# Kernel tuning notes

Measured on AMD Instinct MI355X. Metric: run time of the kernel, lower is better.

The kernel has to match this reference:

```python
import jax, jax.numpy as jnp
import numpy as np

H = 8              # n_heads
N_PER_GRAPH = 64   # nodes per graph (equal-sized graphs)


def setup_inputs() -> dict:
    key = jax.random.key(0)
    ks = jax.random.split(key, 5)
    total, D = 65536, 512
    x = jax.random.normal(ks[0], (total, D), dtype=jnp.float32)
    batch = jnp.arange(total, dtype=jnp.int64) // N_PER_GRAPH  # sorted graph ids
    s = 1.0 / np.sqrt(D).astype(np.float32)
    # nn.MultiheadAttention packed in-proj (xavier-ish uniform) + zero bias
    in_proj_w = jax.random.uniform(ks[1], (3 * D, D), jnp.float32, -s, s)
    in_proj_b = jnp.zeros((3 * D,), jnp.float32)
    out_proj_w = jax.random.uniform(ks[2], (D, D), jnp.float32, -s, s)
    out_proj_b = jnp.zeros((D,), jnp.float32)
    gate_w = jax.random.uniform(ks[3], (1, D), jnp.float32, -s, s)
    gate_b = jnp.zeros((1,), jnp.float32)
    return {"x": x, "batch": batch, "in_proj_w": in_proj_w, "in_proj_b": in_proj_b,
            "out_proj_w": out_proj_w, "out_proj_b": out_proj_b,
            "gate_w": gate_w, "gate_b": gate_b}


def reference(x, batch, in_proj_w, in_proj_b, out_proj_w, out_proj_b, gate_w, gate_b):
    total, D = x.shape
    G = total // N_PER_GRAPH
    hd = D // H
    xg = x.reshape(G, N_PER_GRAPH, D)                       # [G, N, D]
    # packed qkv projection (torch: x @ in_proj_w.T + in_proj_b)
    qkv = jnp.einsum('gnd,ed->gne', xg, in_proj_w) + in_proj_b
    q, k, v = jnp.split(qkv, 3, axis=-1)
    def to_heads(t):
        return t.reshape(G, N_PER_GRAPH, H, hd).transpose(0, 2, 1, 3)  # [G, H, N, hd]
    q, k, v = to_heads(q), to_heads(k), to_heads(v)
    scores = jnp.einsum('ghnd,ghmd->ghnm', q, k) * (1.0 / np.sqrt(hd))
    attn = jax.nn.softmax(scores, axis=-1)
    ctx = jnp.einsum('ghnm,ghmd->ghnd', attn, v)
    ctx = ctx.transpose(0, 2, 1, 3).reshape(G, N_PER_GRAPH, D)
    attn_out = jnp.einsum('gnd,ed->gne', ctx, out_proj_w) + out_proj_b  # [G, N, D]
    gates = jax.nn.sigmoid(jnp.einsum('gnd,od->gno', attn_out, gate_w) + gate_b)
    return (attn_out * gates).sum(axis=1)                   # [G, D]
```

## Files before the change

### kernel.cpp

```cpp
#include <hip/hip_runtime.h>
#include <stdint.h>


typedef __attribute__((ext_vector_type(8))) short short8;
typedef __attribute__((ext_vector_type(4))) float f32x4;

#define D_ 512

#define WQKV_OFF   0u
#define WO_OFF     1572864u
#define UPART_OFF  2097152u
#define U_OFF      2129920u
#define C0_OFF     2131968u
#define SG_OFF     2132032u
#define WCTX_OFF   2136128u

__device__ __forceinline__ unsigned short f2bf(float f) {
    union { float f; unsigned int u; } t; t.f = f;
    unsigned int u = t.u;
    return (unsigned short)((u + 0x7FFFu + ((u >> 16) & 1u)) >> 16);
}
__device__ __forceinline__ unsigned pack2(float a, float b) {
    return (unsigned)f2bf(a) | ((unsigned)f2bf(b) << 16);
}

__global__ __launch_bounds__(256)
void convert_weights(const float* __restrict__ wqkv, const float* __restrict__ wo,
                     unsigned short* __restrict__ wbf) {
    const int i4 = blockIdx.x * 256 + threadIdx.x;
    float4 v;
    if (i4 < 196608) v = *(const float4*)(wqkv + (size_t)i4 * 4);
    else             v = *(const float4*)(wo   + (size_t)(i4 - 196608) * 4);
    uint2 p; p.x = pack2(v.x, v.y); p.y = pack2(v.z, v.w);
    *(uint2*)(wbf + (size_t)i4 * 4) = p;
}

__global__ __launch_bounds__(256)
void compute_u_partial(const float* __restrict__ wo, const float* __restrict__ gw,
                       float* __restrict__ upart) {
    const int b = blockIdx.x;
    const int t = threadIdx.x;
    float a0 = 0.f, a1 = 0.f;
    #pragma unroll 4
    for (int e = b * 32; e < b * 32 + 32; ++e) {
        const float ge = gw[e];
        a0 += wo[(size_t)e * 512 + t]       * ge;
        a1 += wo[(size_t)e * 512 + t + 256] * ge;
    }
    upart[b * 512 + t] = a0; upart[b * 512 + t + 256] = a1;
}

__global__ __launch_bounds__(256)
void finalize_u(const float* __restrict__ upart, const float* __restrict__ bo,
                const float* __restrict__ gw, const float* __restrict__ gb,
                float* __restrict__ u, float* __restrict__ c0) {
    const int t = threadIdx.x;
    float s0 = 0.f, s1 = 0.f;
    #pragma unroll
    for (int b = 0; b < 16; ++b) { s0 += upart[b*512 + t]; s1 += upart[b*512 + t + 256]; }
    u[t] = s0; u[t + 256] = s1;
    __shared__ float rb[256];
    rb[t] = bo[t] * gw[t] + bo[t + 256] * gw[t + 256];
    __syncthreads();
    for (int s = 128; s > 0; s >>= 1) { if (t < s) rb[t] += rb[t + s]; __syncthreads(); }
    if (t == 0) c0[0] = rb[0] + gb[0];
}

union U8 { unsigned u[4]; short8 s; };

__global__ __launch_bounds__(512, 2)
void attn_ctx_kernel(const float* __restrict__ x,
                     const unsigned short* __restrict__ wqkv,
                     const float* __restrict__ bqkv,
                     const float* __restrict__ u,
                     const float* __restrict__ c0,
                     unsigned short* __restrict__ wctx_ws,
                     float* __restrict__ sumgate)
{
    __shared__ unsigned short xs[64][520];
    __shared__ unsigned short scr[8][64][72];
    __shared__ float logitp[8][64];
    __shared__ float gatev[64];

    const int g    = blockIdx.x;
    const int tid  = threadIdx.x;
    const int w    = tid >> 6;
    const int lane = tid & 63;
    const int l15  = lane & 15;
    const int quad = lane >> 4;

    #pragma unroll
    for (int i = 0; i < 16; ++i) {
        int idx = tid + i * 512;
        int row = idx >> 7;
        int c4  = idx & 127;
        float4 v = *(const float4*)(x + ((size_t)(g*64 + row))*512 + c4*4);
        uint2 p; p.x = pack2(v.x, v.y); p.y = pack2(v.z, v.w);
        *(uint2*)(&xs[row][c4*4]) = p;
    }
    __syncthreads();

    const int h = w;
    unsigned short (*S)[72] = scr[w];

    U8 qA[4][2], kB[4][2];
    #pragma unroll
    for (int dt = 0; dt < 4; ++dt) {
        f32x4 aq[4], ak[4], av[4];
        #pragma unroll
        for (int nt = 0; nt < 4; ++nt) {
            aq[nt] = (f32x4){0.f,0.f,0.f,0.f};
            ak[nt] = (f32x4){0.f,0.f,0.f,0.f};
            av[nt] = (f32x4){0.f,0.f,0.f,0.f};
        }
        const unsigned short* wq = wqkv + (size_t)(          h*64 + dt*16 + l15) * 512;
        const unsigned short* wk = wqkv + (size_t)( 512 +    h*64 + dt*16 + l15) * 512;
        const unsigned short* wv = wqkv + (size_t)(1024 +    h*64 + dt*16 + l15) * 512;
        #pragma unroll 4
        for (int ks = 0; ks < 16; ++ks) {
            const int col = ks*32 + quad*8;
            short8 a0 = *(const short8*)(wq + col);
            short8 a1 = *(const short8*)(wk + col);
            short8 a2 = *(const short8*)(wv + col);
            #pragma unroll
            for (int nt = 0; nt < 4; ++nt) {
                short8 b = *(const short8*)(&xs[nt*16 + l15][col]);
                aq[nt] = __builtin_amdgcn_mfma_f32_16x16x32_bf16(a0, b, aq[nt], 0,0,0);
                ak[nt] = __builtin_amdgcn_mfma_f32_16x16x32_bf16(a1, b, ak[nt], 0,0,0);
                av[nt] = __builtin_amdgcn_mfma_f32_16x16x32_bf16(a2, b, av[nt], 0,0,0);
            }
        }
        float bq[4], bk2[4], bv2[4];
        #pragma unroll
        for (int r = 0; r < 4; ++r) {
            bq[r]  = bqkv[          h*64 + dt*16 + quad*4 + r];
            bk2[r] = bqkv[ 512 +    h*64 + dt*16 + quad*4 + r];
            bv2[r] = bqkv[1024 +    h*64 + dt*16 + quad*4 + r];
        }
        const bool take = ((quad >> 1) == (dt & 1));
        const int  ks2  = dt >> 1;
        #pragma unroll
        for (int nt = 0; nt < 4; ++nt) {
            unsigned q01 = pack2(aq[nt][0]+bq[0],  aq[nt][1]+bq[1]);
            unsigned q23 = pack2(aq[nt][2]+bq[2],  aq[nt][3]+bq[3]);
            unsigned k01 = pack2(ak[nt][0]+bk2[0], ak[nt][1]+bk2[1]);
            unsigned k23 = pack2(ak[nt][2]+bk2[2], ak[nt][3]+bk2[3]);
            #pragma unroll
            for (int j = 0; j < 4; ++j) {
                int srcl = ((quad & 1)*2 + (j >> 1))*16 + l15;
                unsigned tq = (unsigned)__shfl((int)((j & 1) ? q23 : q01), srcl);
                unsigned tk = (unsigned)__shfl((int)((j & 1) ? k23 : k01), srcl);
                if (take) { qA[nt][ks2].u[j] = tq; kB[nt][ks2].u[j] = tk; }
            }
            #pragma unroll
            for (int r = 0; r < 4; ++r)
                S[dt*16 + quad*4 + r][nt*16 + l15] = f2bf(av[nt][r] + bv2[r]);
        }
    }

    f32x4 sacc[4][4];
    #pragma unroll
    for (int a = 0; a < 4; ++a)
        #pragma unroll
        for (int b = 0; b < 4; ++b) sacc[a][b] = (f32x4){0.f,0.f,0.f,0.f};
    #pragma unroll
    for (int ks2 = 0; ks2 < 2; ++ks2)
        #pragma unroll
        for (int a = 0; a < 4; ++a)
            #pragma unroll
            for (int b = 0; b < 4; ++b)
                sacc[a][b] = __builtin_amdgcn_mfma_f32_16x16x32_bf16(
                                 qA[a][ks2].s, kB[b][ks2].s, sacc[a][b], 0,0,0);

    #pragma unroll
    for (int a = 0; a < 4; ++a) {
        #pragma unroll
        for (int r = 0; r < 4; ++r) {
            float m0 = -1e30f;
            #pragma unroll
            for (int b = 0; b < 4; ++b) { sacc[a][b][r] *= 0.125f; m0 = fmaxf(m0, sacc[a][b][r]); }
            m0 = fmaxf(m0, __shfl_xor(m0, 1));
            m0 = fmaxf(m0, __shfl_xor(m0, 2));
            m0 = fmaxf(m0, __shfl_xor(m0, 4));
            m0 = fmaxf(m0, __shfl_xor(m0, 8));
            float s = 0.f;
            #pragma unroll
            for (int b = 0; b < 4; ++b) { float e = __expf(sacc[a][b][r] - m0); sacc[a][b][r] = e; s += e; }
            s += __shfl_xor(s, 1); s += __shfl_xor(s, 2); s += __shfl_xor(s, 4); s += __shfl_xor(s, 8);
            float inv = 1.0f / s;
            #pragma unroll
            for (int b = 0; b < 4; ++b) sacc[a][b][r] *= inv;
        }
    }

    U8 vA[4][2];
    #pragma unroll
    for (int dtile = 0; dtile < 4; ++dtile)
        #pragma unroll
        for (int ks2 = 0; ks2 < 2; ++ks2)
            vA[dtile][ks2].s = *(const short8*)(&S[dtile*16 + l15][ks2*32 + quad*8]);

    #pragma unroll
    for (int a = 0; a < 4; ++a)
        #pragma unroll
        for (int b = 0; b < 4; ++b)
            #pragma unroll
            for (int r = 0; r < 4; ++r)
                S[a*16 + quad*4 + r][b*16 + l15] = f2bf(sacc[a][b][r]);

    U8 pB[4][2];
    #pragma unroll
    for (int a = 0; a < 4; ++a)
        #pragma unroll
        for (int ks2 = 0; ks2 < 2; ++ks2)
            pB[a][ks2].s = *(const short8*)(&S[a*16 + l15][ks2*32 + quad*8]);

    f32x4 cacc[4][4];
    #pragma unroll
    for (int dtile = 0; dtile < 4; ++dtile)
        #pragma unroll
        for (int a = 0; a < 4; ++a) cacc[dtile][a] = (f32x4){0.f,0.f,0.f,0.f};
    #pragma unroll
    for (int ks2 = 0; ks2 < 2; ++ks2)
        #pragma unroll
        for (int dtile = 0; dtile < 4; ++dtile)
            #pragma unroll
            for (int a = 0; a < 4; ++a)
                cacc[dtile][a] = __builtin_amdgcn_mfma_f32_16x16x32_bf16(
                                     vA[dtile][ks2].s, pB[a][ks2].s, cacc[dtile][a], 0,0,0);

    {
        float uv[4][4];
        #pragma unroll
        for (int dtile = 0; dtile < 4; ++dtile)
            #pragma unroll
            for (int r = 0; r < 4; ++r)
                uv[dtile][r] = u[h*64 + dtile*16 + quad*4 + r];
        #pragma unroll
        for (int a = 0; a < 4; ++a) {
            float s = 0.f;
            #pragma unroll
            for (int dtile = 0; dtile < 4; ++dtile)
                #pragma unroll
                for (int r = 0; r < 4; ++r)
                    s += cacc[dtile][a][r] * uv[dtile][r];
            s += __shfl_xor(s, 16); s += __shfl_xor(s, 32);
            if (quad == 0) logitp[w][a*16 + l15] = s;
        }
    }
    __syncthreads();

    if (tid < 64) {
        float lg = c0[0];
        #pragma unroll
        for (int ww = 0; ww < 8; ++ww) lg += logitp[ww][tid];
        float gt = 1.0f / (1.0f + __expf(-lg));
        gatev[tid] = gt;
        float s = gt;
        s += __shfl_xor(s, 1);  s += __shfl_xor(s, 2);  s += __shfl_xor(s, 4);
        s += __shfl_xor(s, 8);  s += __shfl_xor(s, 16); s += __shfl_xor(s, 32);
        if (tid == 0) sumgate[g] = s;
    }
    __syncthreads();

    {
        float gv[4];
        #pragma unroll
        for (int a = 0; a < 4; ++a) gv[a] = gatev[a*16 + l15];
        #pragma unroll
        for (int dtile = 0; dtile < 4; ++dtile) {
            float sr[4];
            #pragma unroll
            for (int r = 0; r < 4; ++r) {
                float s = cacc[dtile][0][r]*gv[0] + cacc[dtile][1][r]*gv[1]
                        + cacc[dtile][2][r]*gv[2] + cacc[dtile][3][r]*gv[3];
                s += __shfl_xor(s, 1); s += __shfl_xor(s, 2);
                s += __shfl_xor(s, 4); s += __shfl_xor(s, 8);
                sr[r] = s;
            }
            if (l15 == 0) {
                uint2 pk; pk.x = pack2(sr[0], sr[1]); pk.y = pack2(sr[2], sr[3]);
                *(uint2*)(wctx_ws + (size_t)g*512 + h*64 + dtile*16 + quad*4) = pk;
            }
        }
    }
}

__global__ __launch_bounds__(256, 4)
void outproj_kernel(const unsigned short* __restrict__ wo_bf,
                    const unsigned short* __restrict__ wctx_bf,
                    const float* __restrict__ bo,
                    const float* __restrict__ sumgate,
                    float* __restrict__ out)
{
    const int tid  = threadIdx.x;
    const int w    = tid >> 6;
    const int lane = tid & 63;
    const int l15  = lane & 15;
    const int quad = lane >> 4;
    const int g0   = blockIdx.x * 32;

    f32x4 oac[8][2];
    #pragma unroll
    for (int et = 0; et < 8; ++et)
        #pragma unroll
        for (int mt = 0; mt < 2; ++mt)
            oac[et][mt] = (f32x4){0.f,0.f,0.f,0.f};

    #pragma unroll 4
    for (int ks = 0; ks < 16; ++ks) {
        const int col = ks*32 + quad*8;
        short8 a0 = *(const short8*)(wctx_bf + (size_t)(g0 + l15)*D_      + col);
        short8 a1 = *(const short8*)(wctx_bf + (size_t)(g0 + 16 + l15)*D_ + col);
        #pragma unroll
        for (int et = 0; et < 8; ++et) {
            short8 b = *(const short8*)(wo_bf + (size_t)(w*128 + et*16 + l15)*D_ + col);
            oac[et][0] = __builtin_amdgcn_mfma_f32_16x16x32_bf16(a0, b, oac[et][0], 0,0,0);
            oac[et][1] = __builtin_amdgcn_mfma_f32_16x16x32_bf16(a1, b, oac[et][1], 0,0,0);
        }
    }
    #pragma unroll
    for (int et = 0; et < 8; ++et) {
        const int e = w*128 + et*16 + l15;
        const float bov = bo[e];
        #pragma unroll
        for (int mt = 0; mt < 2; ++mt)
            #pragma unroll
            for (int r = 0; r < 4; ++r) {
                const int gg = g0 + mt*16 + quad*4 + r;
                out[(size_t)gg*D_ + e] = oac[et][mt][r] + sumgate[gg] * bov;
            }
    }
}

extern "C" void kernel_launch(void* const* d_in, const int* in_sizes, int n_in,
                              void* d_out, int out_size, void* d_ws, size_t ws_size,
                              hipStream_t stream) {
    const float* x    = (const float*)d_in[0];
    const float* wqkv = (const float*)d_in[2];
    const float* bqkv = (const float*)d_in[3];
    const float* wo   = (const float*)d_in[4];
    const float* bo   = (const float*)d_in[5];
    const float* gw   = (const float*)d_in[6];
    const float* gb   = (const float*)d_in[7];
    float* out = (float*)d_out;

    char* ws = (char*)d_ws;
    unsigned short* wqkv_bf = (unsigned short*)(ws + WQKV_OFF);
    unsigned short* wo_bf   = (unsigned short*)(ws + WO_OFF);
    float*          upart   = (float*)(ws + UPART_OFF);
    float*          u_ws    = (float*)(ws + U_OFF);
    float*          c0_ws   = (float*)(ws + C0_OFF);
    float*          sg_ws   = (float*)(ws + SG_OFF);
    unsigned short* wctx_ws = (unsigned short*)(ws + WCTX_OFF);

    const int total = in_sizes[0] / D_;
    const int G     = total / 64;

    hipLaunchKernelGGL(convert_weights,   dim3(1024), dim3(256), 0, stream, wqkv, wo, wqkv_bf);
    hipLaunchKernelGGL(compute_u_partial, dim3(16),   dim3(256), 0, stream, wo, gw, upart);
    hipLaunchKernelGGL(finalize_u,        dim3(1),    dim3(256), 0, stream, upart, bo, gw, gb, u_ws, c0_ws);
    hipLaunchKernelGGL(attn_ctx_kernel,   dim3(G),    dim3(512), 0, stream,
                       x, wqkv_bf, bqkv, u_ws, c0_ws, wctx_ws, sg_ws);
    hipLaunchKernelGGL(outproj_kernel,    dim3(G/32), dim3(256), 0, stream,
                       wo_bf, wctx_ws, bo, sg_ws, out);
}
```

Measured before the change: 444.9 us.

## Split attention per head across two waves, fuse prep kernels, widen outproj grid

The attention kernel now runs 1024 threads per graph with two waves per head. Each wave computes half the query rows, and the two waves swap K fragments through shared memory. The gate-vector reduction (u, c0) moves into the attention kernel prologue, and the u-partial computation is folded into the weight-conversion launch, cutting the launch count from five to three. The out-projection grid gains a second dimension that splits output columns four ways, which raises block count and lowers per-thread accumulators, at the cost of reloading the wctx tiles once per column block and adding extra barriers inside the attention kernel.

```diff
diff --git a/kernel.cpp b/kernel.cpp
--- a/kernel.cpp
+++ b/kernel.cpp
@@ -10,8 +10,6 @@
 #define WQKV_OFF   0u
 #define WO_OFF     1572864u
 #define UPART_OFF  2097152u
-#define U_OFF      2129920u
-#define C0_OFF     2131968u
 #define SG_OFF     2132032u
 #define WCTX_OFF   2136128u
 
@@ -26,7 +24,21 @@
 
 __global__ __launch_bounds__(256)
 void convert_weights(const float* __restrict__ wqkv, const float* __restrict__ wo,
-                     unsigned short* __restrict__ wbf) {
+                     unsigned short* __restrict__ wbf,
+                     const float* __restrict__ gw, float* __restrict__ upart) {
+    if (blockIdx.x >= 1024) {
+        const int b = blockIdx.x - 1024;
+        const int t = threadIdx.x;
+        float a0 = 0.f, a1 = 0.f;
+        #pragma unroll 4
+        for (int e = b * 32; e < b * 32 + 32; ++e) {
+            const float ge = gw[e];
+            a0 += wo[(size_t)e * 512 + t]       * ge;
+            a1 += wo[(size_t)e * 512 + t + 256] * ge;
+        }
+        upart[b * 512 + t] = a0; upart[b * 512 + t + 256] = a1;
+        return;
+    }
     const int i4 = blockIdx.x * 256 + threadIdx.x;
     float4 v;
     if (i4 < 196608) v = *(const float4*)(wqkv + (size_t)i4 * 4);
@@ -35,51 +47,24 @@
     *(uint2*)(wbf + (size_t)i4 * 4) = p;
 }
 
-__global__ __launch_bounds__(256)
-void compute_u_partial(const float* __restrict__ wo, const float* __restrict__ gw,
-                       float* __restrict__ upart) {
-    const int b = blockIdx.x;
-    const int t = threadIdx.x;
-    float a0 = 0.f, a1 = 0.f;
-    #pragma unroll 4
-    for (int e = b * 32; e < b * 32 + 32; ++e) {
-        const float ge = gw[e];
-        a0 += wo[(size_t)e * 512 + t]       * ge;
-        a1 += wo[(size_t)e * 512 + t + 256] * ge;
-    }
-    upart[b * 512 + t] = a0; upart[b * 512 + t + 256] = a1;
-}
-
-__global__ __launch_bounds__(256)
-void finalize_u(const float* __restrict__ upart, const float* __restrict__ bo,
-                const float* __restrict__ gw, const float* __restrict__ gb,
-                float* __restrict__ u, float* __restrict__ c0) {
-    const int t = threadIdx.x;
-    float s0 = 0.f, s1 = 0.f;
-    #pragma unroll
-    for (int b = 0; b < 16; ++b) { s0 += upart[b*512 + t]; s1 += upart[b*512 + t + 256]; }
-    u[t] = s0; u[t + 256] = s1;
-    __shared__ float rb[256];
-    rb[t] = bo[t] * gw[t] + bo[t + 256] * gw[t + 256];
-    __syncthreads();
-    for (int s = 128; s > 0; s >>= 1) { if (t < s) rb[t] += rb[t + s]; __syncthreads(); }
-    if (t == 0) c0[0] = rb[0] + gb[0];
-}
-
 union U8 { unsigned u[4]; short8 s; };
 
-__global__ __launch_bounds__(512, 2)
+__global__ __launch_bounds__(1024, 4)
 void attn_ctx_kernel(const float* __restrict__ x,
                      const unsigned short* __restrict__ wqkv,
                      const float* __restrict__ bqkv,
-                     const float* __restrict__ u,
-                     const float* __restrict__ c0,
+                     const float* __restrict__ upart,
+                     const float* __restrict__ bo,
+                     const float* __restrict__ gw,
+                     const float* __restrict__ gb,
                      unsigned short* __restrict__ wctx_ws,
                      float* __restrict__ sumgate)
 {
-    __shared__ unsigned short xs[64][520];
-    __shared__ unsigned short scr[8][64][72];
-    __shared__ float logitp[8][64];
+    __shared__ __align__(16) unsigned short xs[64][520];
+    __shared__ __align__(16) unsigned short scr[8][64][72];
+    __shared__ float logitp[16][64];
+    __shared__ float u_s[512];
+    __shared__ float c0_s;
     __shared__ float gatev[64];
 
     const int g    = blockIdx.x;
@@ -88,30 +73,45 @@
     const int lane = tid & 63;
     const int l15  = lane & 15;
     const int quad = lane >> 4;
-
-    #pragma unroll
-    for (int i = 0; i < 16; ++i) {
-        int idx = tid + i * 512;
+    const int h    = w >> 1;
+    const int q2   = w & 1;
+
+    #pragma unroll
+    for (int i = 0; i < 8; ++i) {
+        int idx = tid + i * 1024;
         int row = idx >> 7;
         int c4  = idx & 127;
         float4 v = *(const float4*)(x + ((size_t)(g*64 + row))*512 + c4*4);
         uint2 p; p.x = pack2(v.x, v.y); p.y = pack2(v.z, v.w);
         *(uint2*)(&xs[row][c4*4]) = p;
     }
-    __syncthreads();
-
-    const int h = w;
-    unsigned short (*S)[72] = scr[w];
-
-    U8 qA[4][2], kB[4][2];
+    if (tid < 512) {
+        float s = 0.f;
+        #pragma unroll
+        for (int b = 0; b < 16; ++b) s += upart[b*512 + tid];
+        u_s[tid] = s;
+    } else if (tid < 576) {
+        const int j = tid - 512;
+        float s = 0.f;
+        #pragma unroll
+        for (int i = 0; i < 8; ++i) s += bo[j*8 + i] * gw[j*8 + i];
+        s += __shfl_xor(s, 1);  s += __shfl_xor(s, 2);  s += __shfl_xor(s, 4);
+        s += __shfl_xor(s, 8);  s += __shfl_xor(s, 16); s += __shfl_xor(s, 32);
+        if (j == 0) c0_s = s + gb[0];
+    }
+    __syncthreads();
+
+    unsigned short (*S)[72] = scr[h];
+
+    U8 qA[2][2], kB[2][2];
     #pragma unroll
     for (int dt = 0; dt < 4; ++dt) {
-        f32x4 aq[4], ak[4], av[4];
-        #pragma unroll
-        for (int nt = 0; nt < 4; ++nt) {
-            aq[nt] = (f32x4){0.f,0.f,0.f,0.f};
-            ak[nt] = (f32x4){0.f,0.f,0.f,0.f};
-            av[nt] = (f32x4){0.f,0.f,0.f,0.f};
+        f32x4 aq[2], ak[2], av[2];
+        #pragma unroll
+        for (int n = 0; n < 2; ++n) {
+            aq[n] = (f32x4){0.f,0.f,0.f,0.f};
+            ak[n] = (f32x4){0.f,0.f,0.f,0.f};
+            av[n] = (f32x4){0.f,0.f,0.f,0.f};
         }
         const unsigned short* wq = wqkv + (size_t)(          h*64 + dt*16 + l15) * 512;
         const unsigned short* wk = wqkv + (size_t)( 512 +    h*64 + dt*16 + l15) * 512;
@@ -123,11 +123,11 @@
             short8 a1 = *(const short8*)(wk + col);
             short8 a2 = *(const short8*)(wv + col);
             #pragma unroll
-            for (int nt = 0; nt < 4; ++nt) {
-                short8 b = *(const short8*)(&xs[nt*16 + l15][col]);
-                aq[nt] = __builtin_amdgcn_mfma_f32_16x16x32_bf16(a0, b, aq[nt], 0,0,0);
-                ak[nt] = __builtin_amdgcn_mfma_f32_16x16x32_bf16(a1, b, ak[nt], 0,0,0);
-                av[nt] = __builtin_amdgcn_mfma_f32_16x16x32_bf16(a2, b, av[nt], 0,0,0);
+            for (int n = 0; n < 2; ++n) {
+                short8 b = *(const short8*)(&xs[(q2*2 + n)*16 + l15][col]);
+                aq[n] = __builtin_amdgcn_mfma_f32_16x16x32_bf16(a0, b, aq[n], 0,0,0);
+                ak[n] = __builtin_amdgcn_mfma_f32_16x16x32_bf16(a1, b, ak[n], 0,0,0);
+                av[n] = __builtin_amdgcn_mfma_f32_16x16x32_bf16(a2, b, av[n], 0,0,0);
             }
         }
         float bq[4], bk2[4], bv2[4];
@@ -140,110 +140,134 @@
         const bool take = ((quad >> 1) == (dt & 1));
         const int  ks2  = dt >> 1;
         #pragma unroll
-        for (int nt = 0; nt < 4; ++nt) {
-            unsigned q01 = pack2(aq[nt][0]+bq[0],  aq[nt][1]+bq[1]);
-            unsigned q23 = pack2(aq[nt][2]+bq[2],  aq[nt][3]+bq[3]);
-            unsigned k01 = pack2(ak[nt][0]+bk2[0], ak[nt][1]+bk2[1]);
-            unsigned k23 = pack2(ak[nt][2]+bk2[2], ak[nt][3]+bk2[3]);
+        for (int n = 0; n < 2; ++n) {
+            const int nt = q2*2 + n;
+            unsigned q01 = pack2(aq[n][0]+bq[0],  aq[n][1]+bq[1]);
+            unsigned q23 = pack2(aq[n][2]+bq[2],  aq[n][3]+bq[3]);
+            unsigned k01 = pack2(ak[n][0]+bk2[0], ak[n][1]+bk2[1]);
+            unsigned k23 = pack2(ak[n][2]+bk2[2], ak[n][3]+bk2[3]);
             #pragma unroll
             for (int j = 0; j < 4; ++j) {
                 int srcl = ((quad & 1)*2 + (j >> 1))*16 + l15;
                 unsigned tq = (unsigned)__shfl((int)((j & 1) ? q23 : q01), srcl);
                 unsigned tk = (unsigned)__shfl((int)((j & 1) ? k23 : k01), srcl);
-                if (take) { qA[nt][ks2].u[j] = tq; kB[nt][ks2].u[j] = tk; }
+                if (take) { qA[n][ks2].u[j] = tq; kB[n][ks2].u[j] = tk; }
             }
             #pragma unroll
             for (int r = 0; r < 4; ++r)
-                S[dt*16 + quad*4 + r][nt*16 + l15] = f2bf(av[nt][r] + bv2[r]);
-        }
-    }
-
-    f32x4 sacc[4][4];
-    #pragma unroll
-    for (int a = 0; a < 4; ++a)
-        #pragma unroll
-        for (int b = 0; b < 4; ++b) sacc[a][b] = (f32x4){0.f,0.f,0.f,0.f};
+                S[dt*16 + quad*4 + r][nt*16 + l15] = f2bf(av[n][r] + bv2[r]);
+        }
+    }
+
+    __syncthreads();
+
+    U8 vA[2][2];
+    #pragma unroll
+    for (int dl = 0; dl < 2; ++dl)
+        #pragma unroll
+        for (int km = 0; km < 2; ++km)
+            vA[dl][km].s = *(const short8*)(&S[(q2*2 + dl)*16 + l15][km*32 + quad*8]);
+
+    short8* exch = (short8*)(&xs[0][0]);
+    #pragma unroll
+    for (int n = 0; n < 2; ++n)
+        #pragma unroll
+        for (int ks2 = 0; ks2 < 2; ++ks2)
+            exch[(((w*2) + n)*2 + ks2)*64 + lane] = kB[n][ks2].s;
+    __syncthreads();
+    U8 kBo[2][2];
+    #pragma unroll
+    for (int n = 0; n < 2; ++n)
+        #pragma unroll
+        for (int ks2 = 0; ks2 < 2; ++ks2)
+            kBo[n][ks2].s = exch[((((w^1)*2) + n)*2 + ks2)*64 + lane];
+
+    f32x4 sacc[2][4];
+    #pragma unroll
+    for (int al = 0; al < 2; ++al)
+        #pragma unroll
+        for (int bl = 0; bl < 4; ++bl) sacc[al][bl] = (f32x4){0.f,0.f,0.f,0.f};
     #pragma unroll
     for (int ks2 = 0; ks2 < 2; ++ks2)
         #pragma unroll
-        for (int a = 0; a < 4; ++a)
-            #pragma unroll
-            for (int b = 0; b < 4; ++b)
-                sacc[a][b] = __builtin_amdgcn_mfma_f32_16x16x32_bf16(
-                                 qA[a][ks2].s, kB[b][ks2].s, sacc[a][b], 0,0,0);
-
-    #pragma unroll
-    for (int a = 0; a < 4; ++a) {
+        for (int al = 0; al < 2; ++al) {
+            #pragma unroll
+            for (int n = 0; n < 2; ++n) {
+                sacc[al][n]   = __builtin_amdgcn_mfma_f32_16x16x32_bf16(
+                                    qA[al][ks2].s, kB[n][ks2].s,  sacc[al][n],   0,0,0);
+                sacc[al][2+n] = __builtin_amdgcn_mfma_f32_16x16x32_bf16(
+                                    qA[al][ks2].s, kBo[n][ks2].s, sacc[al][2+n], 0,0,0);
+            }
+        }
+
+    #pragma unroll
+    for (int al = 0; al < 2; ++al) {
         #pragma unroll
         for (int r = 0; r < 4; ++r) {
             float m0 = -1e30f;
             #pragma unroll
-            for (int b = 0; b < 4; ++b) { sacc[a][b][r] *= 0.125f; m0 = fmaxf(m0, sacc[a][b][r]); }
+            for (int bl = 0; bl < 4; ++bl) { sacc[al][bl][r] *= 0.125f; m0 = fmaxf(m0, sacc[al][bl][r]); }
             m0 = fmaxf(m0, __shfl_xor(m0, 1));
             m0 = fmaxf(m0, __shfl_xor(m0, 2));
             m0 = fmaxf(m0, __shfl_xor(m0, 4));
             m0 = fmaxf(m0, __shfl_xor(m0, 8));
             float s = 0.f;
             #pragma unroll
-            for (int b = 0; b < 4; ++b) { float e = __expf(sacc[a][b][r] - m0); sacc[a][b][r] = e; s += e; }
+            for (int bl = 0; bl < 4; ++bl) { float e = __expf(sacc[al][bl][r] - m0); sacc[al][bl][r] = e; s += e; }
             s += __shfl_xor(s, 1); s += __shfl_xor(s, 2); s += __shfl_xor(s, 4); s += __shfl_xor(s, 8);
             float inv = 1.0f / s;
             #pragma unroll
-            for (int b = 0; b < 4; ++b) sacc[a][b][r] *= inv;
-        }
-    }
-
-    U8 vA[4][2];
-    #pragma unroll
-    for (int dtile = 0; dtile < 4; ++dtile)
-        #pragma unroll
-        for (int ks2 = 0; ks2 < 2; ++ks2)
-            vA[dtile][ks2].s = *(const short8*)(&S[dtile*16 + l15][ks2*32 + quad*8]);
-
+            for (int bl = 0; bl < 4; ++bl) sacc[al][bl][r] *= inv;
+        }
+    }
+
+    #pragma unroll
+    for (int al = 0; al < 2; ++al)
+        #pragma unroll
+        for (int bl = 0; bl < 4; ++bl) {
+            const int bg = (bl < 2 ? q2*2 : 2 - q2*2) + (bl & 1);
+            #pragma unroll
+            for (int r = 0; r < 4; ++r)
+                S[(q2*2 + al)*16 + quad*4 + r][bg*16 + l15] = f2bf(sacc[al][bl][r]);
+        }
+    __syncthreads();
+
+    U8 pB[4][2];
     #pragma unroll
     for (int a = 0; a < 4; ++a)
         #pragma unroll
-        for (int b = 0; b < 4; ++b)
+        for (int km = 0; km < 2; ++km)
+            pB[a][km].s = *(const short8*)(&S[a*16 + l15][km*32 + quad*8]);
+
+    f32x4 cacc[2][4];
+    #pragma unroll
+    for (int dl = 0; dl < 2; ++dl)
+        #pragma unroll
+        for (int a = 0; a < 4; ++a) cacc[dl][a] = (f32x4){0.f,0.f,0.f,0.f};
+    #pragma unroll
+    for (int km = 0; km < 2; ++km)
+        #pragma unroll
+        for (int dl = 0; dl < 2; ++dl)
+            #pragma unroll
+            for (int a = 0; a < 4; ++a)
+                cacc[dl][a] = __builtin_amdgcn_mfma_f32_16x16x32_bf16(
+                                  vA[dl][km].s, pB[a][km].s, cacc[dl][a], 0,0,0);
+
+    {
+        float uv[2][4];
+        #pragma unroll
+        for (int dl = 0; dl < 2; ++dl)
             #pragma unroll
             for (int r = 0; r < 4; ++r)
-                S[a*16 + quad*4 + r][b*16 + l15] = f2bf(sacc[a][b][r]);
-
-    U8 pB[4][2];
-    #pragma unroll
-    for (int a = 0; a < 4; ++a)
-        #pragma unroll
-        for (int ks2 = 0; ks2 < 2; ++ks2)
-            pB[a][ks2].s = *(const short8*)(&S[a*16 + l15][ks2*32 + quad*8]);
-
-    f32x4 cacc[4][4];
-    #pragma unroll
-    for (int dtile = 0; dtile < 4; ++dtile)
-        #pragma unroll
-        for (int a = 0; a < 4; ++a) cacc[dtile][a] = (f32x4){0.f,0.f,0.f,0.f};
-    #pragma unroll
-    for (int ks2 = 0; ks2 < 2; ++ks2)
-        #pragma unroll
-        for (int dtile = 0; dtile < 4; ++dtile)
-            #pragma unroll
-            for (int a = 0; a < 4; ++a)
-                cacc[dtile][a] = __builtin_amdgcn_mfma_f32_16x16x32_bf16(
-                                     vA[dtile][ks2].s, pB[a][ks2].s, cacc[dtile][a], 0,0,0);
-
-    {
-        float uv[4][4];
-        #pragma unroll
-        for (int dtile = 0; dtile < 4; ++dtile)
-            #pragma unroll
-            for (int r = 0; r < 4; ++r)
-                uv[dtile][r] = u[h*64 + dtile*16 + quad*4 + r];
+                uv[dl][r] = u_s[h*64 + (q2*2 + dl)*16 + quad*4 + r];
         #pragma unroll
         for (int a = 0; a < 4; ++a) {
             float s = 0.f;
             #pragma unroll
-            for (int dtile = 0; dtile < 4; ++dtile)
+            for (int dl = 0; dl < 2; ++dl)
                 #pragma unroll
                 for (int r = 0; r < 4; ++r)
-                    s += cacc[dtile][a][r] * uv[dtile][r];
+                    s += cacc[dl][a][r] * uv[dl][r];
             s += __shfl_xor(s, 16); s += __shfl_xor(s, 32);
             if (quad == 0) logitp[w][a*16 + l15] = s;
         }
@@ -251,9 +275,9 @@
     __syncthreads();
 
     if (tid < 64) {
-        float lg = c0[0];
-        #pragma unroll
-        for (int ww = 0; ww < 8; ++ww) lg += logitp[ww][tid];
+        float lg = c0_s;
+        #pragma unroll
+        for (int ww = 0; ww < 16; ++ww) lg += logitp[ww][tid];
         float gt = 1.0f / (1.0f + __expf(-lg));
         gatev[tid] = gt;
         float s = gt;
@@ -268,19 +292,19 @@
         #pragma unroll
         for (int a = 0; a < 4; ++a) gv[a] = gatev[a*16 + l15];
         #pragma unroll
-        for (int dtile = 0; dtile < 4; ++dtile) {
+        for (int dl = 0; dl < 2; ++dl) {
             float sr[4];
             #pragma unroll
             for (int r = 0; r < 4; ++r) {
-                float s = cacc[dtile][0][r]*gv[0] + cacc[dtile][1][r]*gv[1]
-                        + cacc[dtile][2][r]*gv[2] + cacc[dtile][3][r]*gv[3];
+                float s = cacc[dl][0][r]*gv[0] + cacc[dl][1][r]*gv[1]
+                        + cacc[dl][2][r]*gv[2] + cacc[dl][3][r]*gv[3];
                 s += __shfl_xor(s, 1); s += __shfl_xor(s, 2);
                 s += __shfl_xor(s, 4); s += __shfl_xor(s, 8);
                 sr[r] = s;
             }
             if (l15 == 0) {
                 uint2 pk; pk.x = pack2(sr[0], sr[1]); pk.y = pack2(sr[2], sr[3]);
-                *(uint2*)(wctx_ws + (size_t)g*512 + h*64 + dtile*16 + quad*4) = pk;
+                *(uint2*)(wctx_ws + (size_t)g*512 + h*64 + (q2*2 + dl)*16 + quad*4) = pk;
             }
         }
     }
@@ -299,10 +323,11 @@
     const int l15  = lane & 15;
     const int quad = lane >> 4;
     const int g0   = blockIdx.x * 32;
-
-    f32x4 oac[8][2];
-    #pragma unroll
-    for (int et = 0; et < 8; ++et)
+    const int e0   = blockIdx.y * 128;
+
+    f32x4 oac[2][2];
+    #pragma unroll
+    for (int et = 0; et < 2; ++et)
         #pragma unroll
         for (int mt = 0; mt < 2; ++mt)
             oac[et][mt] = (f32x4){0.f,0.f,0.f,0.f};
@@ -313,15 +338,15 @@
         short8 a0 = *(const short8*)(wctx_bf + (size_t)(g0 + l15)*D_      + col);
         short8 a1 = *(const short8*)(wctx_bf + (size_t)(g0 + 16 + l15)*D_ + col);
         #pragma unroll
-        for (int et = 0; et < 8; ++et) {
-            short8 b = *(const short8*)(wo_bf + (size_t)(w*128 + et*16 + l15)*D_ + col);
+        for (int et = 0; et < 2; ++et) {
+            short8 b = *(const short8*)(wo_bf + (size_t)(e0 + w*32 + et*16 + l15)*D_ + col);
             oac[et][0] = __builtin_amdgcn_mfma_f32_16x16x32_bf16(a0, b, oac[et][0], 0,0,0);
             oac[et][1] = __builtin_amdgcn_mfma_f32_16x16x32_bf16(a1, b, oac[et][1], 0,0,0);
         }
     }
     #pragma unroll
-    for (int et = 0; et < 8; ++et) {
-        const int e = w*128 + et*16 + l15;
+    for (int et = 0; et < 2; ++et) {
+        const int e = e0 + w*32 + et*16 + l15;
         const float bov = bo[e];
         #pragma unroll
         for (int mt = 0; mt < 2; ++mt)
@@ -349,19 +374,16 @@
     unsigned short* wqkv_bf = (unsigned short*)(ws + WQKV_OFF);
     unsigned short* wo_bf   = (unsigned short*)(ws + WO_OFF);
     float*          upart   = (float*)(ws + UPART_OFF);
-    float*          u_ws    = (float*)(ws + U_OFF);
-    float*          c0_ws   = (float*)(ws + C0_OFF);
     float*          sg_ws   = (float*)(ws + SG_OFF);
     unsigned short* wctx_ws = (unsigned short*)(ws + WCTX_OFF);
 
     const int total = in_sizes[0] / D_;
     const int G     = total / 64;
 
-    hipLaunchKernelGGL(convert_weights,   dim3(1024), dim3(256), 0, stream, wqkv, wo, wqkv_bf);
-    hipLaunchKernelGGL(compute_u_partial, dim3(16),   dim3(256), 0, stream, wo, gw, upart);
-    hipLaunchKernelGGL(finalize_u,        dim3(1),    dim3(256), 0, stream, upart, bo, gw, gb, u_ws, c0_ws);
-    hipLaunchKernelGGL(attn_ctx_kernel,   dim3(G),    dim3(512), 0, stream,
-                       x, wqkv_bf, bqkv, u_ws, c0_ws, wctx_ws, sg_ws);
-    hipLaunchKernelGGL(outproj_kernel,    dim3(G/32), dim3(256), 0, stream,
+    hipLaunchKernelGGL(convert_weights, dim3(1040), dim3(256), 0, stream,
+                       wqkv, wo, wqkv_bf, gw, upart);
+    hipLaunchKernelGGL(attn_ctx_kernel, dim3(G), dim3(1024), 0, stream,
+                       x, wqkv_bf, bqkv, upart, bo, gw, gb, wctx_ws, sg_ws);
+    hipLaunchKernelGGL(outproj_kernel, dim3(G/32, 4), dim3(256), 0, stream,
                        wo_bf, wctx_ws, bo, sg_ws, out);
 }
```

Measured after the change: 585.9 us. 1.32x slower.

## Pre-convert x to bf16 and read it directly from global in attention kernel

Applied to the files above, without the earlier changes.

Adds a pass that converts x to bf16 in workspace, merged with the weight-conversion and gate-vector kernels into one launch. A new attention kernel reads bf16 x rows straight from global memory into MFMA operands instead of staging fp32 x through a large shared tile, which frees LDS and targets 4 waves per EU. The out-projection grid is also split across output columns for more parallelism. The trade is an extra full read and write of x, and a fallback path is kept for when the workspace is too small.

```diff
diff --git a/kernel.cpp b/kernel.cpp
--- a/kernel.cpp
+++ b/kernel.cpp
@@ -14,6 +14,7 @@
 #define C0_OFF     2131968u
 #define SG_OFF     2132032u
 #define WCTX_OFF   2136128u
+#define XBF_OFF    3184704u
 
 __device__ __forceinline__ unsigned short f2bf(float f) {
     union { float f; unsigned int u; } t; t.f = f;
@@ -25,21 +26,31 @@
 }
 
 __global__ __launch_bounds__(256)
-void convert_weights(const float* __restrict__ wqkv, const float* __restrict__ wo,
-                     unsigned short* __restrict__ wbf) {
-    const int i4 = blockIdx.x * 256 + threadIdx.x;
-    float4 v;
-    if (i4 < 196608) v = *(const float4*)(wqkv + (size_t)i4 * 4);
-    else             v = *(const float4*)(wo   + (size_t)(i4 - 196608) * 4);
-    uint2 p; p.x = pack2(v.x, v.y); p.y = pack2(v.z, v.w);
-    *(uint2*)(wbf + (size_t)i4 * 4) = p;
-}
-
-__global__ __launch_bounds__(256)
-void compute_u_partial(const float* __restrict__ wo, const float* __restrict__ gw,
-                       float* __restrict__ upart) {
-    const int b = blockIdx.x;
-    const int t = threadIdx.x;
+void convert_all(const float* __restrict__ x, const float* __restrict__ wqkv,
+                 const float* __restrict__ wo,
+                 unsigned short* __restrict__ xbf, unsigned short* __restrict__ wbf,
+                 const float* __restrict__ gw, float* __restrict__ upart,
+                 int nxb)
+{
+    const int bid = blockIdx.x;
+    const int t   = threadIdx.x;
+    if (bid < nxb) {
+        const int i4 = bid * 256 + t;
+        float4 v = *(const float4*)(x + (size_t)i4 * 4);
+        uint2 p; p.x = pack2(v.x, v.y); p.y = pack2(v.z, v.w);
+        *(uint2*)(xbf + (size_t)i4 * 4) = p;
+        return;
+    }
+    if (bid < nxb + 1024) {
+        const int i4 = (bid - nxb) * 256 + t;
+        float4 v;
+        if (i4 < 196608) v = *(const float4*)(wqkv + (size_t)i4 * 4);
+        else             v = *(const float4*)(wo   + (size_t)(i4 - 196608) * 4);
+        uint2 p; p.x = pack2(v.x, v.y); p.y = pack2(v.z, v.w);
+        *(uint2*)(wbf + (size_t)i4 * 4) = p;
+        return;
+    }
+    const int b = bid - (nxb + 1024);
     float a0 = 0.f, a1 = 0.f;
     #pragma unroll 4
     for (int e = b * 32; e < b * 32 + 32; ++e) {
@@ -68,14 +79,234 @@
 
 union U8 { unsigned u[4]; short8 s; };
 
+__global__ __launch_bounds__(512) __attribute__((amdgpu_waves_per_eu(4, 4)))
+void attn_ctx_fast(const unsigned short* __restrict__ xbf,
+                   const unsigned short* __restrict__ wqkv,
+                   const float* __restrict__ bqkv,
+                   const float* __restrict__ u,
+                   const float* __restrict__ c0,
+                   unsigned short* __restrict__ wctx_ws,
+                   float* __restrict__ sumgate)
+{
+    __shared__ __align__(16) unsigned short scr[8][64][72];
+    __shared__ float logitp[8][64];
+    __shared__ float gatev[64];
+
+    const int g    = blockIdx.x;
+    const int tid  = threadIdx.x;
+    const int w    = tid >> 6;
+    const int lane = tid & 63;
+    const int l15  = lane & 15;
+    const int quad = lane >> 4;
+    const int h    = w;
+
+    unsigned short (*S)[72] = scr[w];
+
+    const unsigned short* xrow0 = xbf + (size_t)(g*64 +  0 + l15) * 512;
+    const unsigned short* xrow1 = xbf + (size_t)(g*64 + 16 + l15) * 512;
+    const unsigned short* xrow2 = xbf + (size_t)(g*64 + 32 + l15) * 512;
+    const unsigned short* xrow3 = xbf + (size_t)(g*64 + 48 + l15) * 512;
+
+    U8 qA[4][2], kB[4][2];
+    #pragma unroll
+    for (int dt = 0; dt < 4; ++dt) {
+        f32x4 aq[4], ak[4], av[4];
+        #pragma unroll
+        for (int nt = 0; nt < 4; ++nt) {
+            aq[nt] = (f32x4){0.f,0.f,0.f,0.f};
+            ak[nt] = (f32x4){0.f,0.f,0.f,0.f};
+            av[nt] = (f32x4){0.f,0.f,0.f,0.f};
+        }
+        const unsigned short* wq = wqkv + (size_t)(          h*64 + dt*16 + l15) * 512;
+        const unsigned short* wk = wqkv + (size_t)( 512 +    h*64 + dt*16 + l15) * 512;
+        const unsigned short* wv = wqkv + (size_t)(1024 +    h*64 + dt*16 + l15) * 512;
+        #pragma unroll 4
+        for (int ks = 0; ks < 16; ++ks) {
+            const int col = ks*32 + quad*8;
+            short8 a0 = *(const short8*)(wq + col);
+            short8 a1 = *(const short8*)(wk + col);
+            short8 a2 = *(const short8*)(wv + col);
+            short8 b0 = *(const short8*)(xrow0 + col);
+            short8 b1 = *(const short8*)(xrow1 + col);
+            short8 b2 = *(const short8*)(xrow2 + col);
+            short8 b3 = *(const short8*)(xrow3 + col);
+            aq[0] = __builtin_amdgcn_mfma_f32_16x16x32_bf16(a0, b0, aq[0], 0,0,0);
+            ak[0] = __builtin_amdgcn_mfma_f32_16x16x32_bf16(a1, b0, ak[0], 0,0,0);
+            av[0] = __builtin_amdgcn_mfma_f32_16x16x32_bf16(a2, b0, av[0], 0,0,0);
+            aq[1] = __builtin_amdgcn_mfma_f32_16x16x32_bf16(a0, b1, aq[1], 0,0,0);
+            ak[1] = __builtin_amdgcn_mfma_f32_16x16x32_bf16(a1, b1, ak[1], 0,0,0);
+            av[1] = __builtin_amdgcn_mfma_f32_16x16x32_bf16(a2, b1, av[1], 0,0,0);
+            aq[2] = __builtin_amdgcn_mfma_f32_16x16x32_bf16(a0, b2, aq[2], 0,0,0);
+            ak[2] = __builtin_amdgcn_mfma_f32_16x16x32_bf16(a1, b2, ak[2], 0,0,0);
+            av[2] = __builtin_amdgcn_mfma_f32_16x16x32_bf16(a2, b2, av[2], 0,0,0);
+            aq[3] = __builtin_amdgcn_mfma_f32_16x16x32_bf16(a0, b3, aq[3], 0,0,0);
+            ak[3] = __builtin_amdgcn_mfma_f32_16x16x32_bf16(a1, b3, ak[3], 0,0,0);
+            av[3] = __builtin_amdgcn_mfma_f32_16x16x32_bf16(a2, b3, av[3], 0,0,0);
+        }
+        float bq[4], bk2[4], bv2[4];
+        #pragma unroll
+        for (int r = 0; r < 4; ++r) {
+            bq[r]  = bqkv[          h*64 + dt*16 + quad*4 + r];
+            bk2[r] = bqkv[ 512 +    h*64 + dt*16 + quad*4 + r];
+            bv2[r] = bqkv[1024 +    h*64 + dt*16 + quad*4 + r];
+        }
+        const bool take = ((quad >> 1) == (dt & 1));
+        const int  ks2  = dt >> 1;
+        #pragma unroll
+        for (int nt = 0; nt < 4; ++nt) {
+            unsigned q01 = pack2(aq[nt][0]+bq[0],  aq[nt][1]+bq[1]);
+            unsigned q23 = pack2(aq[nt][2]+bq[2],  aq[nt][3]+bq[3]);
+            unsigned k01 = pack2(ak[nt][0]+bk2[0], ak[nt][1]+bk2[1]);
+            unsigned k23 = pack2(ak[nt][2]+bk2[2], ak[nt][3]+bk2[3]);
+            #pragma unroll
+            for (int j = 0; j < 4; ++j) {
+                int srcl = ((quad & 1)*2 + (j >> 1))*16 + l15;
+                unsigned tq = (unsigned)__shfl((int)((j & 1) ? q23 : q01), srcl);
+                unsigned tk = (unsigned)__shfl((int)((j & 1) ? k23 : k01), srcl);
+                if (take) { qA[nt][ks2].u[j] = tq; kB[nt][ks2].u[j] = tk; }
+            }
+            #pragma unroll
+            for (int r = 0; r < 4; ++r)
+                S[dt*16 + quad*4 + r][nt*16 + l15] = f2bf(av[nt][r] + bv2[r]);
+        }
+    }
+
+    f32x4 sacc[4][4];
+    #pragma unroll
+    for (int a = 0; a < 4; ++a)
+        #pragma unroll
+        for (int b = 0; b < 4; ++b) sacc[a][b] = (f32x4){0.f,0.f,0.f,0.f};
+    #pragma unroll
+    for (int ks2 = 0; ks2 < 2; ++ks2)
+        #pragma unroll
+        for (int a = 0; a < 4; ++a)
+            #pragma unroll
+            for (int b = 0; b < 4; ++b)
+                sacc[a][b] = __builtin_amdgcn_mfma_f32_16x16x32_bf16(
+                                 qA[a][ks2].s, kB[b][ks2].s, sacc[a][b], 0,0,0);
+
+    #pragma unroll
+    for (int a = 0; a < 4; ++a) {
+        #pragma unroll
+        for (int r = 0; r < 4; ++r) {
+            float m0 = -1e30f;
+            #pragma unroll
+            for (int b = 0; b < 4; ++b) { sacc[a][b][r] *= 0.125f; m0 = fmaxf(m0, sacc[a][b][r]); }
+            m0 = fmaxf(m0, __shfl_xor(m0, 1));
+            m0 = fmaxf(m0, __shfl_xor(m0, 2));
+            m0 = fmaxf(m0, __shfl_xor(m0, 4));
+            m0 = fmaxf(m0, __shfl_xor(m0, 8));
+            float s = 0.f;
+            #pragma unroll
+            for (int b = 0; b < 4; ++b) { float e = __expf(sacc[a][b][r] - m0); sacc[a][b][r] = e; s += e; }
+            s += __shfl_xor(s, 1); s += __shfl_xor(s, 2); s += __shfl_xor(s, 4); s += __shfl_xor(s, 8);
+            float inv = 1.0f / s;
+            #pragma unroll
+            for (int b = 0; b < 4; ++b) sacc[a][b][r] *= inv;
+        }
+    }
+
+    U8 vA[4][2];
+    #pragma unroll
+    for (int dtile = 0; dtile < 4; ++dtile)
+        #pragma unroll
+        for (int ks2 = 0; ks2 < 2; ++ks2)
+            vA[dtile][ks2].s = *(const short8*)(&S[dtile*16 + l15][ks2*32 + quad*8]);
+
+    #pragma unroll
+    for (int a = 0; a < 4; ++a)
+        #pragma unroll
+        for (int b = 0; b < 4; ++b)
+            #pragma unroll
+            for (int r = 0; r < 4; ++r)
+                S[a*16 + quad*4 + r][b*16 + l15] = f2bf(sacc[a][b][r]);
+
+    U8 pB[4][2];
+    #pragma unroll
+    for (int a = 0; a < 4; ++a)
+        #pragma unroll
+        for (int ks2 = 0; ks2 < 2; ++ks2)
+            pB[a][ks2].s = *(const short8*)(&S[a*16 + l15][ks2*32 + quad*8]);
+
+    f32x4 cacc[4][4];
+    #pragma unroll
+    for (int dtile = 0; dtile < 4; ++dtile)
+        #pragma unroll
+        for (int a = 0; a < 4; ++a) cacc[dtile][a] = (f32x4){0.f,0.f,0.f,0.f};
+    #pragma unroll
+    for (int ks2 = 0; ks2 < 2; ++ks2)
+        #pragma unroll
+        for (int dtile = 0; dtile < 4; ++dtile)
+            #pragma unroll
+            for (int a = 0; a < 4; ++a)
+                cacc[dtile][a] = __builtin_amdgcn_mfma_f32_16x16x32_bf16(
+                                     vA[dtile][ks2].s, pB[a][ks2].s, cacc[dtile][a], 0,0,0);
+
+    {
+        float uv[4][4];
+        #pragma unroll
+        for (int dtile = 0; dtile < 4; ++dtile)
+            #pragma unroll
+            for (int r = 0; r < 4; ++r)
+                uv[dtile][r] = u[h*64 + dtile*16 + quad*4 + r];
+        #pragma unroll
+        for (int a = 0; a < 4; ++a) {
+            float s = 0.f;
+            #pragma unroll
+            for (int dtile = 0; dtile < 4; ++dtile)
+                #pragma unroll
+                for (int r = 0; r < 4; ++r)
+                    s += cacc[dtile][a][r] * uv[dtile][r];
+            s += __shfl_xor(s, 16); s += __shfl_xor(s, 32);
+            if (quad == 0) logitp[w][a*16 + l15] = s;
+        }
+    }
+    __syncthreads();
+
+    if (tid < 64) {
+        float lg = c0[0];
+        #pragma unroll
+        for (int ww = 0; ww < 8; ++ww) lg += logitp[ww][tid];
+        float gt = 1.0f / (1.0f + __expf(-lg));
+        gatev[tid] = gt;
+        float s = gt;
+        s += __shfl_xor(s, 1);  s += __shfl_xor(s, 2);  s += __shfl_xor(s, 4);
+        s += __shfl_xor(s, 8);  s += __shfl_xor(s, 16); s += __shfl_xor(s, 32);
+        if (tid == 0) sumgate[g] = s;
+    }
+    __syncthreads();
+
+    {
+        float gv[4];
+        #pragma unroll
+        for (int a = 0; a < 4; ++a) gv[a] = gatev[a*16 + l15];
+        #pragma unroll
+        for (int dtile = 0; dtile < 4; ++dtile) {
+            float sr[4];
+            #pragma unroll
+            for (int r = 0; r < 4; ++r) {
+                float s = cacc[dtile][0][r]*gv[0] + cacc[dtile][1][r]*gv[1]
+                        + cacc[dtile][2][r]*gv[2] + cacc[dtile][3][r]*gv[3];
+                s += __shfl_xor(s, 1); s += __shfl_xor(s, 2);
+                s += __shfl_xor(s, 4); s += __shfl_xor(s, 8);
+                sr[r] = s;
+            }
+            if (l15 == 0) {
+                uint2 pk; pk.x = pack2(sr[0], sr[1]); pk.y = pack2(sr[2], sr[3]);
+                *(uint2*)(wctx_ws + (size_t)g*512 + h*64 + dtile*16 + quad*4) = pk;
+            }
+        }
+    }
+}
+
 __global__ __launch_bounds__(512, 2)
-void attn_ctx_kernel(const float* __restrict__ x,
-                     const unsigned short* __restrict__ wqkv,
-                     const float* __restrict__ bqkv,
-                     const float* __restrict__ u,
-                     const float* __restrict__ c0,
-                     unsigned short* __restrict__ wctx_ws,
-                     float* __restrict__ sumgate)
+void attn_ctx_v6(const float* __restrict__ x,
+                 const unsigned short* __restrict__ wqkv,
+                 const float* __restrict__ bqkv,
+                 const float* __restrict__ u,
+                 const float* __restrict__ c0,
+                 unsigned short* __restrict__ wctx_ws,
+                 float* __restrict__ sumgate)
 {
     __shared__ unsigned short xs[64][520];
     __shared__ unsigned short scr[8][64][72];
@@ -298,38 +529,23 @@
     const int lane = tid & 63;
     const int l15  = lane & 15;
     const int quad = lane >> 4;
-    const int g0   = blockIdx.x * 32;
-
-    f32x4 oac[8][2];
-    #pragma unroll
-    for (int et = 0; et < 8; ++et)
-        #pragma unroll
-        for (int mt = 0; mt < 2; ++mt)
-            oac[et][mt] = (f32x4){0.f,0.f,0.f,0.f};
-
+    const int g0   = blockIdx.x * 16;
+    const int e0   = blockIdx.y * 64;
+
+    f32x4 oac = (f32x4){0.f,0.f,0.f,0.f};
     #pragma unroll 4
     for (int ks = 0; ks < 16; ++ks) {
         const int col = ks*32 + quad*8;
-        short8 a0 = *(const short8*)(wctx_bf + (size_t)(g0 + l15)*D_      + col);
-        short8 a1 = *(const short8*)(wctx_bf + (size_t)(g0 + 16 + l15)*D_ + col);
-        #pragma unroll
-        for (int et = 0; et < 8; ++et) {
-            short8 b = *(const short8*)(wo_bf + (size_t)(w*128 + et*16 + l15)*D_ + col);
-            oac[et][0] = __builtin_amdgcn_mfma_f32_16x16x32_bf16(a0, b, oac[et][0], 0,0,0);
-            oac[et][1] = __builtin_amdgcn_mfma_f32_16x16x32_bf16(a1, b, oac[et][1], 0,0,0);
-        }
-    }
-    #pragma unroll
-    for (int et = 0; et < 8; ++et) {
-        const int e = w*128 + et*16 + l15;
-        const float bov = bo[e];
-        #pragma unroll
-        for (int mt = 0; mt < 2; ++mt)
-            #pragma unroll
-            for (int r = 0; r < 4; ++r) {
-                const int gg = g0 + mt*16 + quad*4 + r;
-                out[(size_t)gg*D_ + e] = oac[et][mt][r] + sumgate[gg] * bov;
-            }
+        short8 a = *(const short8*)(wctx_bf + (size_t)(g0 + l15)*D_ + col);
+        short8 b = *(const short8*)(wo_bf + (size_t)(e0 + w*16 + l15)*D_ + col);
+        oac = __builtin_amdgcn_mfma_f32_16x16x32_bf16(a, b, oac, 0,0,0);
+    }
+    const int e = e0 + w*16 + l15;
+    const float bov = bo[e];
+    #pragma unroll
+    for (int r = 0; r < 4; ++r) {
+        const int gg = g0 + quad*4 + r;
+        out[(size_t)gg*D_ + e] = oac[r] + sumgate[gg] * bov;
     }
 }
 
@@ -353,15 +569,26 @@
     float*          c0_ws   = (float*)(ws + C0_OFF);
     float*          sg_ws   = (float*)(ws + SG_OFF);
     unsigned short* wctx_ws = (unsigned short*)(ws + WCTX_OFF);
+    unsigned short* xbf     = (unsigned short*)(ws + XBF_OFF);
 
     const int total = in_sizes[0] / D_;
     const int G     = total / 64;
 
-    hipLaunchKernelGGL(convert_weights,   dim3(1024), dim3(256), 0, stream, wqkv, wo, wqkv_bf);
-    hipLaunchKernelGGL(compute_u_partial, dim3(16),   dim3(256), 0, stream, wo, gw, upart);
-    hipLaunchKernelGGL(finalize_u,        dim3(1),    dim3(256), 0, stream, upart, bo, gw, gb, u_ws, c0_ws);
-    hipLaunchKernelGGL(attn_ctx_kernel,   dim3(G),    dim3(512), 0, stream,
-                       x, wqkv_bf, bqkv, u_ws, c0_ws, wctx_ws, sg_ws);
-    hipLaunchKernelGGL(outproj_kernel,    dim3(G/32), dim3(256), 0, stream,
+    const size_t need_fast = (size_t)XBF_OFF + (size_t)total * 512 * 2;
+    const bool   fast      = ws_size >= need_fast;
+    const int    nxb       = fast ? total / 2 : 0;
+
+    hipLaunchKernelGGL(convert_all, dim3(nxb + 1040), dim3(256), 0, stream,
+                       x, wqkv, wo, xbf, wqkv_bf, gw, upart, nxb);
+    hipLaunchKernelGGL(finalize_u, dim3(1), dim3(256), 0, stream,
+                       upart, bo, gw, gb, u_ws, c0_ws);
+    if (fast) {
+        hipLaunchKernelGGL(attn_ctx_fast, dim3(G), dim3(512), 0, stream,
+                           xbf, wqkv_bf, bqkv, u_ws, c0_ws, wctx_ws, sg_ws);
+    } else {
+        hipLaunchKernelGGL(attn_ctx_v6, dim3(G), dim3(512), 0, stream,
+                           x, wqkv_bf, bqkv, u_ws, c0_ws, wctx_ws, sg_ws);
+    }
+    hipLaunchKernelGGL(outproj_kernel, dim3(G/16, 8), dim3(256), 0, stream,
                        wo_bf, wctx_ws, bo, sg_ws, out);
 }
```

Result: slower. 676.2 us (+52.0%).
